# Kernel optimization log

Hardware: AMD Instinct MI355X
Metric: run time of the kernel (lower is better)

Reference implementation:

```python
import jax, jax.numpy as jnp
import numpy as np

B, L, E, IN_A, IN_B, OUT = 32, 4096, 1024, 1024, 1024, 64
CACHE_LEN = 2048


def setup_inputs() -> dict:
    key = jax.random.key(0)
    ks = jax.random.split(key, 8)
    s = lambda n: 1.0 / np.sqrt(n)
    return {
        "inputA": jax.random.normal(ks[0], (B, IN_A), dtype=jnp.float32),
        "inputB": jax.random.normal(ks[1], (B, IN_B), dtype=jnp.float32),
        "cache": jnp.zeros((B, L, E), dtype=jnp.float32),
        "W1a": jax.random.normal(ks[2], (E, IN_A), dtype=jnp.float32) * s(IN_A),
        "b1a": jax.random.normal(ks[3], (E,), dtype=jnp.float32) * s(IN_A),
        "W1b": jax.random.normal(ks[4], (E, IN_B), dtype=jnp.float32) * s(IN_B),
        "b1b": jax.random.normal(ks[5], (E,), dtype=jnp.float32) * s(IN_B),
        "W2": jax.random.normal(ks[6], (OUT, E), dtype=jnp.float32) * s(E),
        "b2": jax.random.normal(ks[7], (OUT,), dtype=jnp.float32) * s(E),
        "cache_len": CACHE_LEN,
    }


def reference(inputA, inputB, cache, W1a, b1a, W1b, b1b, W2, b2, cache_len):
    # dual small Linear + add -> [B, E]
    vec = inputA @ W1a.T + b1a + inputB @ W1b.T + b1b
    # dynamic-index cache write (torch does this under no_grad)
    new_cache = cache.at[:, cache_len].set(jax.lax.stop_gradient(vec))
    # dynamic-length slice [B, cache_len+1, E], then output projection
    sliced = new_cache[:, : cache_len + 1]
    out = sliced @ W2.T + b2  # [B, cache_len+1, OUT]
    return out, new_cache
```

## Files before the change

### kernel.cpp

```cpp
#include <hip/hip_runtime.h>

#define Bq   32
#define Lq   4096
#define Eq   1024
#define OUTq 64
#define NW   16
#define TG   8

__global__ __launch_bounds__(256) void vec_kernel(
    const float* __restrict__ inA, const float* __restrict__ inB,
    const float* __restrict__ W1a, const float* __restrict__ b1a,
    const float* __restrict__ W1b, const float* __restrict__ b1b,
    float* __restrict__ vec)
{
    int wid  = (blockIdx.x * 256 + threadIdx.x) >> 6;
    int lane = threadIdx.x & 63;
    if (wid >= Eq) return;
    int e = wid;

    const float4* wa4 = (const float4*)(W1a + (size_t)e * Eq);
    const float4* wb4 = (const float4*)(W1b + (size_t)e * Eq);
    float4 wa[4], wb[4];
#pragma unroll
    for (int j = 0; j < 4; ++j) { wa[j] = wa4[lane + 64 * j]; wb[j] = wb4[lane + 64 * j]; }
    float bias = b1a[e] + b1b[e];

#pragma unroll 4
    for (int b = 0; b < Bq; ++b) {
        const float4* a4  = (const float4*)(inA + (size_t)b * Eq);
        const float4* bb4 = (const float4*)(inB + (size_t)b * Eq);
        float acc = 0.f;
#pragma unroll
        for (int j = 0; j < 4; ++j) {
            float4 a = a4[lane + 64 * j];
            acc += wa[j].x * a.x + wa[j].y * a.y + wa[j].z * a.z + wa[j].w * a.w;
            float4 v = bb4[lane + 64 * j];
            acc += wb[j].x * v.x + wb[j].y * v.y + wb[j].z * v.z + wb[j].w * v.w;
        }
#pragma unroll
        for (int s = 32; s; s >>= 1) acc += __shfl_xor(acc, s, 64);
        if (lane == 0) vec[(size_t)b * Eq + e] = acc + bias;
    }
}

__global__ __launch_bounds__(1024, 4) void fused_kernel(
    const float* __restrict__ cache, const float* __restrict__ vec,
    const float* __restrict__ W2, const float* __restrict__ b2,
    float* __restrict__ outp, float* __restrict__ ncache,
    int cache_len, int ngg, int ncg)
{
    const int rows_out = cache_len + 1;
    const int tid = threadIdx.x;
    const int w = tid >> 6, lane = tid & 63;
    const int b   = blockIdx.x >> 3;
    const int blk = blockIdx.x & 7;

    __shared__ float rowbuf[TG][Eq];
    __shared__ float part[NW][TG * 64];

    float4 w2r[16];
#pragma unroll
    for (int j = 0; j < 16; ++j)
        w2r[j] = *(const float4*)(W2 + (size_t)lane * Eq + 64 * w + 4 * j);

    const float bias = b2[tid & 63];

    const int rsub = tid >> 7;
    const int c    = tid & 127;

    const float* cb = cache  + (size_t)b * Lq * Eq;
    float*       nb = ncache + (size_t)b * Lq * Eq;
    const float* vb = vec    + (size_t)b * Eq;

    float4 gld0 = {0,0,0,0}, gld1 = {0,0,0,0}, cld0 = {0,0,0,0}, cld1 = {0,0,0,0};

    auto fetch_g = [&](int g) {
        int t = TG * g + rsub;
        if (g < ngg && t <= cache_len) {
            const float* src = (t == cache_len) ? vb : (cb + (size_t)t * Eq);
            gld0 = *(const float4*)(src + 4 * c);
            gld1 = *(const float4*)(src + 4 * (c + 128));
        }
    };
    auto fetch_c = [&](int cg) {
        int t = rows_out + TG * cg + rsub;
        if (cg < ncg && t < Lq) {
            const float* src = cb + (size_t)t * Eq;
            cld0 = *(const float4*)(src + 4 * c);
            cld1 = *(const float4*)(src + 4 * (c + 128));
        }
    };

    fetch_g(blk);
    fetch_c(blk);

    for (int g = blk; g < ngg; g += 8) {
        int t = TG * g + rsub;
        if (t <= cache_len) {
            float* dst = nb + (size_t)t * Eq;
            *(float4*)(dst + 4 * c)          = gld0;
            *(float4*)(dst + 4 * (c + 128))  = gld1;
            *(float4*)(&rowbuf[rsub][4 * c])         = gld0;
            *(float4*)(&rowbuf[rsub][4 * (c + 128)]) = gld1;
        }
        int tc = rows_out + TG * g + rsub;
        if (g < ncg && tc < Lq) {
            float* dst = nb + (size_t)tc * Eq;
            *(float4*)(dst + 4 * c)         = cld0;
            *(float4*)(dst + 4 * (c + 128)) = cld1;
        }

        fetch_g(g + 8);
        fetch_c(g + 8);

        asm volatile("s_waitcnt lgkmcnt(0)\n\ts_barrier" ::: "memory");

#pragma unroll
        for (int r = 0; r < TG; ++r) {
            float acc = 0.f;
#pragma unroll
            for (int j = 0; j < 16; ++j) {
                float4 rv = *(const float4*)(&rowbuf[r][64 * w + 4 * j]);
                acc += rv.x * w2r[j].x + rv.y * w2r[j].y +
                       rv.z * w2r[j].z + rv.w * w2r[j].w;
            }
            part[w][r * 64 + lane] = acc;
        }

        asm volatile("s_waitcnt lgkmcnt(0)\n\ts_barrier" ::: "memory");

        if (tid < TG * 64) {
            int rr = tid >> 6, o = tid & 63;
            int trow = TG * g + rr;
            if (trow < rows_out) {
                float s = 0.f;
#pragma unroll
                for (int ww = 0; ww < NW; ++ww) s += part[ww][tid];
                outp[((size_t)b * rows_out + trow) * OUTq + o] = s + bias;
            }
        }
    }
}

extern "C" void kernel_launch(void* const* d_in, const int* in_sizes, int n_in,
                              void* d_out, int out_size, void* d_ws, size_t ws_size,
                              hipStream_t stream)
{
    const float* inA   = (const float*)d_in[0];
    const float* inB   = (const float*)d_in[1];
    const float* cache = (const float*)d_in[2];
    const float* W1a   = (const float*)d_in[3];
    const float* b1a   = (const float*)d_in[4];
    const float* W1b   = (const float*)d_in[5];
    const float* b1b   = (const float*)d_in[6];
    const float* W2    = (const float*)d_in[7];
    const float* b2v   = (const float*)d_in[8];

    float* outp = (float*)d_out;
    int rows_out  = (out_size - Bq * Lq * Eq) / (Bq * OUTq);
    int cache_len = rows_out - 1;
    float* ncache = outp + (size_t)Bq * rows_out * OUTq;
    float* vecbuf = (float*)d_ws;

    int ngg = (rows_out + TG - 1) / TG;
    int ncg = (Lq - rows_out + TG - 1) / TG;

    vec_kernel<<<dim3(256), dim3(256), 0, stream>>>(inA, inB, W1a, b1a, W1b, b1b, vecbuf);

    fused_kernel<<<dim3(256), dim3(1024), 0, stream>>>(cache, vecbuf, W2, b2v,
                                                       outp, ncache,
                                                       cache_len, ngg, ncg);
}
```

Baseline: 350.1 us.

## Split cache tail copy into dedicated blocks and use fp16 dot2 for projection

```diff
diff --git a/kernel.cpp b/kernel.cpp
--- a/kernel.cpp
+++ b/kernel.cpp
@@ -7,16 +7,34 @@
 #define NW   16
 #define TG   8
 
+typedef decltype(__builtin_amdgcn_cvt_pkrtz(0.f, 0.f)) h2;
+
+#if defined(__has_builtin)
+#if __has_builtin(__builtin_amdgcn_fdot2)
+#define HAVE_FDOT2 1
+#endif
+#endif
+
+static __device__ __forceinline__ float dot2f(unsigned a, h2 b, float c) {
+    h2 ah = __builtin_bit_cast(h2, a);
+#ifdef HAVE_FDOT2
+    return __builtin_amdgcn_fdot2(ah, b, c, false);
+#else
+    return c + (float)ah[0] * (float)b[0] + (float)ah[1] * (float)b[1];
+#endif
+}
+
+#define LGKM_BARRIER() asm volatile("s_waitcnt lgkmcnt(0)\n\ts_barrier" ::: "memory")
+
 __global__ __launch_bounds__(256) void vec_kernel(
     const float* __restrict__ inA, const float* __restrict__ inB,
     const float* __restrict__ W1a, const float* __restrict__ b1a,
     const float* __restrict__ W1b, const float* __restrict__ b1b,
     float* __restrict__ vec)
 {
-    int wid  = (blockIdx.x * 256 + threadIdx.x) >> 6;
+    int e    = (blockIdx.x * 256 + threadIdx.x) >> 6;
     int lane = threadIdx.x & 63;
-    if (wid >= Eq) return;
-    int e = wid;
+    if (e >= Eq) return;
 
     const float4* wa4 = (const float4*)(W1a + (size_t)e * Eq);
     const float4* wb4 = (const float4*)(W1b + (size_t)e * Eq);
@@ -43,101 +61,129 @@
     }
 }
 
-__global__ __launch_bounds__(1024, 4) void fused_kernel(
+__global__ __launch_bounds__(1024, 8) void mega_kernel(
     const float* __restrict__ cache, const float* __restrict__ vec,
     const float* __restrict__ W2, const float* __restrict__ b2,
-    float* __restrict__ outp, float* __restrict__ ncache,
-    int cache_len, int ngg, int ncg)
+    float* __restrict__ outp, float* __restrict__ ncache, int cache_len)
 {
-    const int rows_out = cache_len + 1;
+    __shared__ unsigned rowbuf[TG][Eq / 2];
+    __shared__ float    part[NW][TG * 64];
+
     const int tid = threadIdx.x;
-    const int w = tid >> 6, lane = tid & 63;
-    const int b   = blockIdx.x >> 3;
-    const int blk = blockIdx.x & 7;
-
-    __shared__ float rowbuf[TG][Eq];
-    __shared__ float part[NW][TG * 64];
-
-    float4 w2r[16];
-#pragma unroll
-    for (int j = 0; j < 16; ++j)
-        w2r[j] = *(const float4*)(W2 + (size_t)lane * Eq + 64 * w + 4 * j);
-
-    const float bias = b2[tid & 63];
-
-    const int rsub = tid >> 7;
-    const int c    = tid & 127;
-
-    const float* cb = cache  + (size_t)b * Lq * Eq;
-    float*       nb = ncache + (size_t)b * Lq * Eq;
-    const float* vb = vec    + (size_t)b * Eq;
-
-    float4 gld0 = {0,0,0,0}, gld1 = {0,0,0,0}, cld0 = {0,0,0,0}, cld1 = {0,0,0,0};
-
-    auto fetch_g = [&](int g) {
-        int t = TG * g + rsub;
-        if (g < ngg && t <= cache_len) {
-            const float* src = (t == cache_len) ? vb : (cb + (size_t)t * Eq);
-            gld0 = *(const float4*)(src + 4 * c);
-            gld1 = *(const float4*)(src + 4 * (c + 128));
-        }
-    };
-    auto fetch_c = [&](int cg) {
-        int t = rows_out + TG * cg + rsub;
-        if (cg < ncg && t < Lq) {
-            const float* src = cb + (size_t)t * Eq;
-            cld0 = *(const float4*)(src + 4 * c);
-            cld1 = *(const float4*)(src + 4 * (c + 128));
-        }
-    };
-
-    fetch_g(blk);
-    fetch_c(blk);
-
-    for (int g = blk; g < ngg; g += 8) {
-        int t = TG * g + rsub;
-        if (t <= cache_len) {
-            float* dst = nb + (size_t)t * Eq;
-            *(float4*)(dst + 4 * c)          = gld0;
-            *(float4*)(dst + 4 * (c + 128))  = gld1;
-            *(float4*)(&rowbuf[rsub][4 * c])         = gld0;
-            *(float4*)(&rowbuf[rsub][4 * (c + 128)]) = gld1;
-        }
-        int tc = rows_out + TG * g + rsub;
-        if (g < ncg && tc < Lq) {
-            float* dst = nb + (size_t)tc * Eq;
-            *(float4*)(dst + 4 * c)         = cld0;
-            *(float4*)(dst + 4 * (c + 128)) = cld1;
-        }
-
-        fetch_g(g + 8);
-        fetch_c(g + 8);
-
-        asm volatile("s_waitcnt lgkmcnt(0)\n\ts_barrier" ::: "memory");
-
-#pragma unroll
-        for (int r = 0; r < TG; ++r) {
-            float acc = 0.f;
-#pragma unroll
-            for (int j = 0; j < 16; ++j) {
-                float4 rv = *(const float4*)(&rowbuf[r][64 * w + 4 * j]);
-                acc += rv.x * w2r[j].x + rv.y * w2r[j].y +
-                       rv.z * w2r[j].z + rv.w * w2r[j].w;
-            }
-            part[w][r * 64 + lane] = acc;
-        }
-
-        asm volatile("s_waitcnt lgkmcnt(0)\n\ts_barrier" ::: "memory");
-
-        if (tid < TG * 64) {
-            int rr = tid >> 6, o = tid & 63;
-            int trow = TG * g + rr;
-            if (trow < rows_out) {
-                float s = 0.f;
-#pragma unroll
-                for (int ww = 0; ww < NW; ++ww) s += part[ww][tid];
-                outp[((size_t)b * rows_out + trow) * OUTq + o] = s + bias;
-            }
+
+    if (blockIdx.x < 256) {
+        const int rows_out = cache_len + 1;
+        const int ngg  = (rows_out + TG - 1) / TG;
+        const int b    = blockIdx.x >> 3;
+        const int slot = blockIdx.x & 7;
+        const int w = tid >> 6, lane = tid & 63;
+        const int rsub = tid >> 7, c = tid & 127;
+
+        h2 w2h[32];
+        const float4* w2p = (const float4*)(W2 + (size_t)lane * Eq + 64 * w);
+#pragma unroll
+        for (int j = 0; j < 16; ++j) {
+            float4 f = w2p[j];
+            w2h[2 * j]     = __builtin_amdgcn_cvt_pkrtz(f.x, f.y);
+            w2h[2 * j + 1] = __builtin_amdgcn_cvt_pkrtz(f.z, f.w);
+        }
+        const float bias = b2[lane];
+
+        const float* cb = cache  + (size_t)b * Lq * Eq;
+        float*       nb = ncache + (size_t)b * Lq * Eq;
+        const float* vb = vec    + (size_t)b * Eq;
+        float*       ob = outp   + (size_t)b * rows_out * OUTq;
+
+        float4 gld0, gld1;
+        auto fetch = [&](int g) {
+            int t = TG * g + rsub;
+            if (g < ngg && t <= cache_len) {
+                const float* src = (t == cache_len) ? vb : (cb + (size_t)t * Eq);
+                gld0 = *(const float4*)(src + 4 * c);
+                gld1 = *(const float4*)(src + 4 * c + 512);
+            }
+        };
+        fetch(slot);
+
+        for (int g = slot; g < ngg; g += 8) {
+            int t = TG * g + rsub;
+            if (t <= cache_len) {
+                float* dst = nb + (size_t)t * Eq;
+                *(float4*)(dst + 4 * c)       = gld0;
+                *(float4*)(dst + 4 * c + 512) = gld1;
+                unsigned u0 = __builtin_bit_cast(unsigned, __builtin_amdgcn_cvt_pkrtz(gld0.x, gld0.y));
+                unsigned u1 = __builtin_bit_cast(unsigned, __builtin_amdgcn_cvt_pkrtz(gld0.z, gld0.w));
+                unsigned u2 = __builtin_bit_cast(unsigned, __builtin_amdgcn_cvt_pkrtz(gld1.x, gld1.y));
+                unsigned u3 = __builtin_bit_cast(unsigned, __builtin_amdgcn_cvt_pkrtz(gld1.z, gld1.w));
+                *(uint2*)(&rowbuf[rsub][2 * c])       = make_uint2(u0, u1);
+                *(uint2*)(&rowbuf[rsub][2 * c + 256]) = make_uint2(u2, u3);
+            }
+            fetch(g + 8);
+
+            LGKM_BARRIER();
+
+#pragma unroll
+            for (int r = 0; r < TG; ++r) {
+                float acc = 0.f;
+                const uint4* rp = (const uint4*)(&rowbuf[r][32 * w]);
+#pragma unroll
+                for (int j = 0; j < 8; ++j) {
+                    uint4 v = rp[j];
+                    acc = dot2f(v.x, w2h[4 * j],     acc);
+                    acc = dot2f(v.y, w2h[4 * j + 1], acc);
+                    acc = dot2f(v.z, w2h[4 * j + 2], acc);
+                    acc = dot2f(v.w, w2h[4 * j + 3], acc);
+                }
+                part[w][r * 64 + lane] = acc;
+            }
+
+            LGKM_BARRIER();
+
+            if (tid < TG * 64) {
+                int rr = tid >> 6;
+                int trow = TG * g + rr;
+                if (trow < rows_out) {
+                    float s = 0.f;
+#pragma unroll
+                    for (int ww = 0; ww < NW; ++ww) s += part[ww][tid];
+                    ob[(size_t)trow * OUTq + lane] = s + bias;
+                }
+            }
+        }
+    } else {
+        const int cb2  = blockIdx.x - 256;
+        const int first = cache_len + 1;
+        const int span  = Lq - first;
+        const int nrows = Bq * span;
+        const int rloc  = tid >> 6;
+        const int lane  = tid & 63;
+
+        const float4* s4 = (const float4*)cache;
+        float4*       d4 = (float4*)ncache;
+
+        int Rcur = cb2 * 16 + rloc;
+        size_t offc = 0;
+        float4 p0, p1, p2, p3;
+        if (Rcur < nrows) {
+            int bb = Rcur / span, tr = first + Rcur - bb * span;
+            offc = ((size_t)bb * Lq + tr) * (Eq / 4) + lane;
+            p0 = s4[offc]; p1 = s4[offc + 64]; p2 = s4[offc + 128]; p3 = s4[offc + 192];
+        }
+#pragma unroll 4
+        for (int i = 0; i < 16; ++i) {
+            int Rnext = Rcur + 4096;
+            size_t offn = 0;
+            float4 n0, n1, n2, n3;
+            if (Rnext < nrows) {
+                int bb = Rnext / span, tr = first + Rnext - bb * span;
+                offn = ((size_t)bb * Lq + tr) * (Eq / 4) + lane;
+                n0 = s4[offn]; n1 = s4[offn + 64]; n2 = s4[offn + 128]; n3 = s4[offn + 192];
+            }
+            if (Rcur < nrows) {
+                d4[offc] = p0; d4[offc + 64] = p1; d4[offc + 128] = p2; d4[offc + 192] = p3;
+            }
+            Rcur = Rnext; offc = offn;
+            p0 = n0; p1 = n1; p2 = n2; p3 = n3;
         }
     }
 }
@@ -162,12 +208,8 @@
     float* ncache = outp + (size_t)Bq * rows_out * OUTq;
     float* vecbuf = (float*)d_ws;
 
-    int ngg = (rows_out + TG - 1) / TG;
-    int ncg = (Lq - rows_out + TG - 1) / TG;
-
     vec_kernel<<<dim3(256), dim3(256), 0, stream>>>(inA, inB, W1a, b1a, W1b, b1b, vecbuf);
 
-    fused_kernel<<<dim3(256), dim3(1024), 0, stream>>>(cache, vecbuf, W2, b2v,
-                                                       outp, ncache,
-                                                       cache_len, ngg, ncg);
-}
+    mega_kernel<<<dim3(512), dim3(1024), 0, stream>>>(cache, vecbuf, W2, b2v,
+                                                      outp, ncache, cache_len);
+}
```

Measured after the change: 394.2 us. +12.6%, slower.

## Use fp16 MFMA for output projection with flattened global row scheduling

Applied to the files above, without the earlier changes.

```diff
diff --git a/kernel.cpp b/kernel.cpp
--- a/kernel.cpp
+++ b/kernel.cpp
@@ -1,11 +1,18 @@
 #include <hip/hip_runtime.h>
+
+typedef _Float16 f16x8 __attribute__((ext_vector_type(8)));
+typedef float    f32x4 __attribute__((ext_vector_type(4)));
 
 #define Bq   32
 #define Lq   4096
 #define Eq   1024
-#define OUTq 64
-#define NW   16
-#define TG   8
+#define ROWS_OUT 2049
+#define TOT_G (Bq * ROWS_OUT)
+#define TOT_C (Bq * (Lq - ROWS_OUT))
+#define NGROUP 4098
+#define GBLK  256
+
+#define LGKM_BARRIER() asm volatile("s_waitcnt lgkmcnt(0)\n\ts_barrier" ::: "memory")
 
 __global__ __launch_bounds__(256) void vec_kernel(
     const float* __restrict__ inA, const float* __restrict__ inB,
@@ -13,10 +20,9 @@
     const float* __restrict__ W1b, const float* __restrict__ b1b,
     float* __restrict__ vec)
 {
-    int wid  = (blockIdx.x * 256 + threadIdx.x) >> 6;
+    int e    = (blockIdx.x * 256 + threadIdx.x) >> 6;
     int lane = threadIdx.x & 63;
-    if (wid >= Eq) return;
-    int e = wid;
+    if (e >= Eq) return;
 
     const float4* wa4 = (const float4*)(W1a + (size_t)e * Eq);
     const float4* wb4 = (const float4*)(W1b + (size_t)e * Eq);
@@ -43,102 +49,117 @@
     }
 }
 
-__global__ __launch_bounds__(1024, 4) void fused_kernel(
+__global__ __launch_bounds__(1024, 4) void mega_kernel(
     const float* __restrict__ cache, const float* __restrict__ vec,
     const float* __restrict__ W2, const float* __restrict__ b2,
-    float* __restrict__ outp, float* __restrict__ ncache,
-    int cache_len, int ngg, int ncg)
+    float* __restrict__ outp, float* __restrict__ ncache)
 {
-    const int rows_out = cache_len + 1;
+    __shared__ _Float16 rowbuf_raw[16 * Eq];
+    __shared__ float    part[12 * 64 * 4];
+
     const int tid = threadIdx.x;
-    const int w = tid >> 6, lane = tid & 63;
-    const int b   = blockIdx.x >> 3;
-    const int blk = blockIdx.x & 7;
+    const int w = tid >> 6, l = tid & 63;
+    const int n = w >> 2, q = w & 3;
+    char* rb = (char*)rowbuf_raw;
 
-    __shared__ float rowbuf[TG][Eq];
-    __shared__ float part[NW][TG * 64];
+    f16x8 bfr[8];
+    {
+        const float* wrow = W2 + (size_t)(16 * n + (l & 15)) * Eq;
+#pragma unroll
+        for (int s = 0; s < 8; ++s) {
+            int k0 = (q * 8 + s) * 32 + (l >> 4) * 8;
+            float4 x = *(const float4*)(wrow + k0);
+            float4 y = *(const float4*)(wrow + k0 + 4);
+            f16x8 v;
+            v[0] = (_Float16)x.x; v[1] = (_Float16)x.y; v[2] = (_Float16)x.z; v[3] = (_Float16)x.w;
+            v[4] = (_Float16)y.x; v[5] = (_Float16)y.y; v[6] = (_Float16)y.z; v[7] = (_Float16)y.w;
+            bfr[s] = v;
+        }
+    }
+    const float bias = b2[16 * n + (l & 15)];
 
-    float4 w2r[16];
+    auto issue_loads = [&](int g, float4 (&gl)[4], float4 (&cl)[4]) {
+        int R = g * 16 + w;
+        int bb = R / ROWS_OUT, t = R - bb * ROWS_OUT;
+        const float* srcG = (t == ROWS_OUT - 1) ? (vec + (size_t)bb * Eq)
+                                                : (cache + ((size_t)bb * Lq + t) * Eq);
+        const float4* s4 = (const float4*)srcG;
 #pragma unroll
-    for (int j = 0; j < 16; ++j)
-        w2r[j] = *(const float4*)(W2 + (size_t)lane * Eq + 64 * w + 4 * j);
-
-    const float bias = b2[tid & 63];
-
-    const int rsub = tid >> 7;
-    const int c    = tid & 127;
-
-    const float* cb = cache  + (size_t)b * Lq * Eq;
-    float*       nb = ncache + (size_t)b * Lq * Eq;
-    const float* vb = vec    + (size_t)b * Eq;
-
-    float4 gld0 = {0,0,0,0}, gld1 = {0,0,0,0}, cld0 = {0,0,0,0}, cld1 = {0,0,0,0};
-
-    auto fetch_g = [&](int g) {
-        int t = TG * g + rsub;
-        if (g < ngg && t <= cache_len) {
-            const float* src = (t == cache_len) ? vb : (cb + (size_t)t * Eq);
-            gld0 = *(const float4*)(src + 4 * c);
-            gld1 = *(const float4*)(src + 4 * (c + 128));
-        }
-    };
-    auto fetch_c = [&](int cg) {
-        int t = rows_out + TG * cg + rsub;
-        if (cg < ncg && t < Lq) {
-            const float* src = cb + (size_t)t * Eq;
-            cld0 = *(const float4*)(src + 4 * c);
-            cld1 = *(const float4*)(src + 4 * (c + 128));
+        for (int j = 0; j < 4; ++j) gl[j] = s4[4 * l + j];
+        if (R < TOT_C) {
+            int cb = R / (Lq - ROWS_OUT), tc = ROWS_OUT + R - cb * (Lq - ROWS_OUT);
+            const float4* c4 = (const float4*)(cache + ((size_t)cb * Lq + tc) * Eq);
+#pragma unroll
+            for (int j = 0; j < 4; ++j) cl[j] = c4[4 * l + j];
         }
     };
 
-    fetch_g(blk);
-    fetch_c(blk);
+    auto body = [&](int g, float4 (&gl)[4], float4 (&cl)[4],
+                    float4 (&gl2)[4], float4 (&cl2)[4]) {
+        if (g + GBLK < NGROUP) issue_loads(g + GBLK, gl2, cl2);
 
-    for (int g = blk; g < ngg; g += 8) {
-        int t = TG * g + rsub;
-        if (t <= cache_len) {
-            float* dst = nb + (size_t)t * Eq;
-            *(float4*)(dst + 4 * c)          = gld0;
-            *(float4*)(dst + 4 * (c + 128))  = gld1;
-            *(float4*)(&rowbuf[rsub][4 * c])         = gld0;
-            *(float4*)(&rowbuf[rsub][4 * (c + 128)]) = gld1;
-        }
-        int tc = rows_out + TG * g + rsub;
-        if (g < ncg && tc < Lq) {
-            float* dst = nb + (size_t)tc * Eq;
-            *(float4*)(dst + 4 * c)         = cld0;
-            *(float4*)(dst + 4 * (c + 128)) = cld1;
+        {
+            int R = g * 16 + w;
+            int bb = R / ROWS_OUT, t = R - bb * ROWS_OUT;
+            float4* d4 = (float4*)(ncache + ((size_t)bb * Lq + t) * Eq);
+#pragma unroll
+            for (int j = 0; j < 4; ++j) d4[4 * l + j] = gl[j];
+            if (R < TOT_C) {
+                int cb = R / (Lq - ROWS_OUT), tc = ROWS_OUT + R - cb * (Lq - ROWS_OUT);
+                float4* c4 = (float4*)(ncache + ((size_t)cb * Lq + tc) * Eq);
+#pragma unroll
+                for (int j = 0; j < 4; ++j) c4[4 * l + j] = cl[j];
+            }
+            f16x8 h0, h1;
+            h0[0] = (_Float16)gl[0].x; h0[1] = (_Float16)gl[0].y;
+            h0[2] = (_Float16)gl[0].z; h0[3] = (_Float16)gl[0].w;
+            h0[4] = (_Float16)gl[1].x; h0[5] = (_Float16)gl[1].y;
+            h0[6] = (_Float16)gl[1].z; h0[7] = (_Float16)gl[1].w;
+            h1[0] = (_Float16)gl[2].x; h1[1] = (_Float16)gl[2].y;
+            h1[2] = (_Float16)gl[2].z; h1[3] = (_Float16)gl[2].w;
+            h1[4] = (_Float16)gl[3].x; h1[5] = (_Float16)gl[3].y;
+            h1[6] = (_Float16)gl[3].z; h1[7] = (_Float16)gl[3].w;
+            int base = w * 2048 + l * 32;
+            int swz  = (w & 7) << 4;
+            *(f16x8*)(rb + (base ^ swz))        = h0;
+            *(f16x8*)(rb + ((base + 16) ^ swz)) = h1;
         }
 
-        fetch_g(g + 8);
-        fetch_c(g + 8);
+        LGKM_BARRIER();
 
-        asm volatile("s_waitcnt lgkmcnt(0)\n\ts_barrier" ::: "memory");
-
+        f32x4 acc = {0.f, 0.f, 0.f, 0.f};
+        {
+            const int m    = l & 15;
+            const int aswz = (m & 7) << 4;
+            const int rbase = m * 2048 + (l >> 4) * 16;
 #pragma unroll
-        for (int r = 0; r < TG; ++r) {
-            float acc = 0.f;
-#pragma unroll
-            for (int j = 0; j < 16; ++j) {
-                float4 rv = *(const float4*)(&rowbuf[r][64 * w + 4 * j]);
-                acc += rv.x * w2r[j].x + rv.y * w2r[j].y +
-                       rv.z * w2r[j].z + rv.w * w2r[j].w;
-            }
-            part[w][r * 64 + lane] = acc;
-        }
-
-        asm volatile("s_waitcnt lgkmcnt(0)\n\ts_barrier" ::: "memory");
-
-        if (tid < TG * 64) {
-            int rr = tid >> 6, o = tid & 63;
-            int trow = TG * g + rr;
-            if (trow < rows_out) {
-                float s = 0.f;
-#pragma unroll
-                for (int ww = 0; ww < NW; ++ww) s += part[ww][tid];
-                outp[((size_t)b * rows_out + trow) * OUTq + o] = s + bias;
+            for (int s = 0; s < 8; ++s) {
+                int sa = q * 8 + s;
+                f16x8 afr = *(const f16x8*)(rb + ((rbase + sa * 64) ^ aswz));
+                acc = __builtin_amdgcn_mfma_f32_16x16x32_f16(afr, bfr[s], acc, 0, 0, 0);
             }
         }
+        if (q) *(f32x4*)&part[((n * 3 + q - 1) * 64 + l) * 4] = acc;
+
+        LGKM_BARRIER();
+
+        if (q == 0) {
+#pragma unroll
+            for (int j = 0; j < 3; ++j)
+                acc += *(const f32x4*)&part[((n * 3 + j) * 64 + l) * 4];
+            int R0 = g * 16 + (l >> 4) * 4;
+            float* op = outp + (size_t)R0 * 64 + 16 * n + (l & 15);
+#pragma unroll
+            for (int r = 0; r < 4; ++r) op[(size_t)r * 64] = acc[r] + bias;
+        }
+    };
+
+    float4 gA[4], cA[4], gB[4], cB[4];
+    int g0 = blockIdx.x;
+    issue_loads(g0, gA, cA);
+    for (int g = g0; g < NGROUP; g += 2 * GBLK) {
+        body(g, gA, cA, gB, cB);
+        if (g + GBLK < NGROUP) body(g + GBLK, gB, cB, gA, cA);
     }
 }
 
@@ -156,18 +177,12 @@
     const float* W2    = (const float*)d_in[7];
     const float* b2v   = (const float*)d_in[8];
 
-    float* outp = (float*)d_out;
-    int rows_out  = (out_size - Bq * Lq * Eq) / (Bq * OUTq);
-    int cache_len = rows_out - 1;
-    float* ncache = outp + (size_t)Bq * rows_out * OUTq;
+    float* outp   = (float*)d_out;
+    float* ncache = outp + (size_t)Bq * ROWS_OUT * 64;
     float* vecbuf = (float*)d_ws;
-
-    int ngg = (rows_out + TG - 1) / TG;
-    int ncg = (Lq - rows_out + TG - 1) / TG;
 
     vec_kernel<<<dim3(256), dim3(256), 0, stream>>>(inA, inB, W1a, b1a, W1b, b1b, vecbuf);
 
-    fused_kernel<<<dim3(256), dim3(1024), 0, stream>>>(cache, vecbuf, W2, b2v,
-                                                       outp, ncache,
-                                                       cache_len, ngg, ncg);
+    mega_kernel<<<dim3(GBLK), dim3(1024), 0, stream>>>(cache, vecbuf, W2, b2v,
+                                                       outp, ncache);
 }
```

Result: slower. 420.9 us (+20.2%).
